# Kernel optimization log

Measured on AMD Instinct MI355X. Metric: run time of the kernel, lower is better.

## Reference

```python
import jax, jax.numpy as jnp
import numpy as np

E = 1024
H = 16
D = E // H  # head_dim = 64
B = 2
S = 2048


def setup_inputs() -> dict:
    key = jax.random.key(0)
    ks = jax.random.split(key, 8)
    sc = 0.02
    return {
        "x": jax.random.normal(ks[0], (B, S, E), jnp.float32),
        "rotation_params": jax.random.normal(ks[1], (E, E), jnp.float32) * sc,
        "entangle_params": jax.random.normal(ks[2], (E, E), jnp.float32) * sc,
        "qkv_w": jax.random.normal(ks[3], (3 * E, E), jnp.float32) * sc,
        "qkv_b": jax.random.normal(ks[4], (3 * E,), jnp.float32) * sc,
        "out_w": jax.random.normal(ks[5], (E, E), jnp.float32) * sc,
        "out_b": jax.random.normal(ks[6], (E,), jnp.float32) * sc,
    }


def reference(x, rotation_params, entangle_params, qkv_w, qkv_b, out_w, out_b):
    b, s, _ = x.shape
    # qkv projection (torch Linear: x @ W.T + b)
    qkv = jnp.einsum('bse,fe->bsf', x, qkv_w) + qkv_b
    q, k, v = jnp.split(qkv, 3, axis=-1)
    # extra rotation / entangle matmuls on q and k
    q = jnp.matmul(q, rotation_params)
    k = jnp.matmul(k, entangle_params)
    # split heads: (b, h, s, d)
    q = q.reshape(b, s, H, D).transpose(0, 2, 1, 3)
    k = k.reshape(b, s, H, D).transpose(0, 2, 1, 3)
    v = v.reshape(b, s, H, D).transpose(0, 2, 1, 3)
    scores = jnp.einsum('bhqd,bhkd->bhqk', q, k) / np.sqrt(D).astype(np.float32)
    attn = jax.nn.softmax(scores, axis=-1)  # dropout p=0.0 -> identity
    out = jnp.einsum('bhqk,bhkd->bhqd', attn, v)
    out = out.transpose(0, 2, 1, 3).reshape(b, s, E)
    out = jnp.einsum('bse,fe->bsf', out, out_w) + out_b
    return out + x
```

## Files before the change

### kernel.cpp

```cpp
#include <hip/hip_runtime.h>

#define US unsigned short
#define UC unsigned char

typedef __bf16 bf16x8 __attribute__((ext_vector_type(8)));
typedef float f32x4 __attribute__((ext_vector_type(4)));
typedef unsigned int u32x4 __attribute__((ext_vector_type(4)));
typedef unsigned short u16x4 __attribute__((ext_vector_type(4)));
typedef unsigned int uint2v __attribute__((ext_vector_type(2)));

#define ALPHA_Q 0.180336880111f

#if __has_builtin(__builtin_amdgcn_exp2f)
#define EXP2F(x) __builtin_amdgcn_exp2f(x)
#else
#define EXP2F(x) __expf(0.69314718f * (x))
#endif

static __device__ __forceinline__ US f2bf(float f) {
    union { float f; unsigned u; } v; v.f = f;
    unsigned r = v.u + 0x7fffu + ((v.u >> 16) & 1u);
    return (US)(r >> 16);
}
static __device__ __forceinline__ float bf2f(US h) {
    union { unsigned u; float f; } v; v.u = ((unsigned)h) << 16;
    return v.f;
}
static __device__ __forceinline__ f32x4 mfma16(bf16x8 a, bf16x8 b, f32x4 c) {
    return __builtin_amdgcn_mfma_f32_16x16x32_bf16(a, b, c, 0, 0, 0);
}
static __device__ __forceinline__ f32x4 mfma_fp8(long long a, long long b, f32x4 c) {
    return __builtin_amdgcn_mfma_f32_16x16x32_fp8_fp8(a, b, c, 0, 0, 0);
}
static __device__ __forceinline__ void gload16(const US* g, US* l) {
    __builtin_amdgcn_global_load_lds(
        (const __attribute__((address_space(1))) void*)g,
        (__attribute__((address_space(3))) void*)l, 16, 0, 0);
}
static __device__ __forceinline__ void gload16b(const UC* g, UC* l) {
    __builtin_amdgcn_global_load_lds(
        (const __attribute__((address_space(1))) void*)g,
        (__attribute__((address_space(3))) void*)l, 16, 0, 0);
}
static __device__ __forceinline__ void stf(float* p, float v) { *p = v; }
static __device__ __forceinline__ void stf(US* p, float v) { *p = f2bf(v); }

__global__ __launch_bounds__(256) void prep(
    const float* __restrict__ x, US* __restrict__ xb,
    const float* __restrict__ qkvw, US* __restrict__ wv,
    const float* __restrict__ outw, US* __restrict__ wo,
    const float* __restrict__ Rm, US* __restrict__ rt,
    const float* __restrict__ Em, US* __restrict__ et,
    US* __restrict__ wqT, US* __restrict__ wkT,
    const float* __restrict__ qkvb, float* __restrict__ b3)
{
    __shared__ float t[64][65];
    const int bx = blockIdx.x;
    if (bx < 6144) {
        int i = bx * 256 + threadIdx.x;
        const float* s; US* d; int j;
        if (i < 1048576) { s = x; d = xb; j = i; }
        else if (i < 1310720) { s = qkvw + (size_t)2048 * 1024; d = wv; j = i - 1048576; }
        else { s = outw; d = wo; j = i - 1310720; }
        f32x4 v = ((const f32x4*)s)[j];
        u16x4 o;
        o.x = f2bf(v.x); o.y = f2bf(v.y); o.z = f2bf(v.z); o.w = f2bf(v.w);
        ((u16x4*)d)[j] = o;
    } else if (bx < 7168) {
        int r = bx - 6144;
        int z = r >> 8, xy = r & 255, tbx = xy & 15, tby = xy >> 4;
        const float* ip; US* op;
        switch (z) {
            case 0: ip = Rm; op = rt; break;
            case 1: ip = Em; op = et; break;
            case 2: ip = qkvw; op = wqT; break;
            default: ip = qkvw + (size_t)1024 * 1024; op = wkT; break;
        }
        int bc = tbx * 64, br = tby * 64;
        int lx = threadIdx.x & 63, y4 = threadIdx.x >> 6;
#pragma unroll
        for (int i = 0; i < 16; ++i) {
            int rr = i * 4 + y4;
            t[rr][lx] = ip[(size_t)(br + rr) * 1024 + bc + lx];
        }
        __syncthreads();
#pragma unroll
        for (int i = 0; i < 16; ++i) {
            int c = i * 4 + y4;
            op[(size_t)(bc + c) * 1024 + br + lx] = f2bf(t[lx][c]);
        }
    } else if (bx < 7296) {
        float (*red)[64] = (float(*)[64])t;
        const int bb = bx - 7168;
        const int tid = threadIdx.x, wave = tid >> 6, lane = tid & 63;
        const int nc = bb & 31, jc = bb >> 5;
        const int n0 = nc * 64, n = n0 + lane;
        const float* M = (n0 < 1024) ? Rm : Em;
        const float* bv = qkvb + ((n0 < 1024) ? 0 : 1024);
        const int nn = (n0 < 1024) ? n : n - 1024;
        float s = 0.f;
        const int j0 = jc * 256 + wave * 64;
#pragma unroll 8
        for (int j = 0; j < 64; ++j)
            s += bv[j0 + j] * M[(size_t)(j0 + j) * 1024 + nn];
        red[wave][lane] = s;
        __syncthreads();
        if (wave == 0) {
            float tt = red[0][lane] + red[1][lane] + red[2][lane] + red[3][lane];
            atomicAdd(&b3[n], (n0 < 1024) ? tt * ALPHA_Q : tt);
        }
    } else {
        int i = (bx - 7296) * 256 + threadIdx.x;
        b3[2048 + i] = qkvb[2048 + i];
    }
}

template <typename TO>
__global__ __launch_bounds__(256) void gemm_nt64(
    const US* __restrict__ A, const US* __restrict__ Bm,
    TO* __restrict__ C, const float* __restrict__ bias,
    const float* __restrict__ resid,
    int M, int N, int K, int lda, int ldb, int ldc)
{
    __shared__ __align__(16) US sA[64 * 32];
    __shared__ __align__(16) US sB[128 * 32];
    const int tid = threadIdx.x;
    const int wave = tid >> 6, lane = tid & 63;
    const int r16 = lane & 15, q4 = lane >> 4;
    const int wm = (wave >> 1) * 32, wn = (wave & 1) * 64;

    const US* aptr = A + (size_t)(blockIdx.x * 64 + wave * 16 + (lane >> 2)) * lda + (lane & 3) * 8;
    const US* bptr = Bm + (size_t)(blockIdx.y * 128 + wave * 32 + (lane >> 2)) * ldb + (lane & 3) * 8;
    US* lA = sA + (wave * 16) * 32;
    US* lB = sB + (wave * 32) * 32;

    f32x4 acc[2][4];
#pragma unroll
    for (int i = 0; i < 2; ++i)
#pragma unroll
        for (int j = 0; j < 4; ++j) acc[i][j] = (f32x4){0.f, 0.f, 0.f, 0.f};

    for (int k0 = 0; k0 < K; k0 += 32) {
        gload16(aptr + k0, lA);
        gload16(bptr + k0, lB);
        gload16(bptr + (size_t)16 * ldb + k0, lB + 16 * 32);
        __syncthreads();
        bf16x8 af[2], bfr[4];
#pragma unroll
        for (int i = 0; i < 2; ++i)
            af[i] = *(const bf16x8*)&sA[(wm + i * 16 + r16) * 32 + q4 * 8];
#pragma unroll
        for (int j = 0; j < 4; ++j)
            bfr[j] = *(const bf16x8*)&sB[(wn + j * 16 + r16) * 32 + q4 * 8];
#pragma unroll
        for (int i = 0; i < 2; ++i)
#pragma unroll
            for (int j = 0; j < 4; ++j) acc[i][j] = mfma16(af[i], bfr[j], acc[i][j]);
        __syncthreads();
    }

#pragma unroll
    for (int j = 0; j < 4; ++j) {
        int col = blockIdx.y * 128 + wn + j * 16 + r16;
        float bv = bias ? bias[col] : 0.f;
#pragma unroll
        for (int i = 0; i < 2; ++i) {
#pragma unroll
            for (int rr = 0; rr < 4; ++rr) {
                int row = blockIdx.x * 64 + wm + i * 16 + q4 * 4 + rr;
                float v = acc[i][j][rr] + bv;
                if (resid) v += resid[(size_t)row * ldc + col];
                stf(&C[(size_t)row * ldc + col], v);
            }
        }
    }
}

__global__ __launch_bounds__(256) void gemm_qkv(
    const US* __restrict__ A, const US* __restrict__ Bm,
    const float* __restrict__ bias,
    US* __restrict__ qk, UC* __restrict__ vt)
{
    __shared__ __align__(16) US sA[64 * 32];
    __shared__ __align__(16) US sB[128 * 32];
    const int tid = threadIdx.x;
    const int wave = tid >> 6, lane = tid & 63;
    const int r16 = lane & 15, q4 = lane >> 4;
    const int wm = (wave >> 1) * 32, wn = (wave & 1) * 64;

    const US* aptr = A + (size_t)(blockIdx.x * 64 + wave * 16 + (lane >> 2)) * 1024 + (lane & 3) * 8;
    const US* bptr = Bm + (size_t)(blockIdx.y * 128 + wave * 32 + (lane >> 2)) * 1024 + (lane & 3) * 8;
    US* lA = sA + (wave * 16) * 32;
    US* lB = sB + (wave * 32) * 32;

    f32x4 acc[2][4];
#pragma unroll
    for (int i = 0; i < 2; ++i)
#pragma unroll
        for (int j = 0; j < 4; ++j) acc[i][j] = (f32x4){0.f, 0.f, 0.f, 0.f};

    for (int k0 = 0; k0 < 1024; k0 += 32) {
        gload16(aptr + k0, lA);
        gload16(bptr + k0, lB);
        gload16(bptr + (size_t)16 * 1024 + k0, lB + 16 * 32);
        __syncthreads();
        bf16x8 af[2], bfr[4];
#pragma unroll
        for (int i = 0; i < 2; ++i)
            af[i] = *(const bf16x8*)&sA[(wm + i * 16 + r16) * 32 + q4 * 8];
#pragma unroll
        for (int j = 0; j < 4; ++j)
            bfr[j] = *(const bf16x8*)&sB[(wn + j * 16 + r16) * 32 + q4 * 8];
#pragma unroll
        for (int i = 0; i < 2; ++i)
#pragma unroll
            for (int j = 0; j < 4; ++j) acc[i][j] = mfma16(af[i], bfr[j], acc[i][j]);
        __syncthreads();
    }

    if (blockIdx.y < 16) {
#pragma unroll
        for (int j = 0; j < 4; ++j) {
            int col = blockIdx.y * 128 + wn + j * 16 + r16;
            float bv = bias[col];
#pragma unroll
            for (int i = 0; i < 2; ++i)
#pragma unroll
                for (int rr = 0; rr < 4; ++rr) {
                    int row = blockIdx.x * 64 + wm + i * 16 + q4 * 4 + rr;
                    qk[(size_t)row * 2048 + col] = f2bf(acc[i][j][rr] + bv);
                }
        }
    } else {
#pragma unroll
        for (int j = 0; j < 4; ++j) {
            int col = blockIdx.y * 128 + wn + j * 16 + r16;
            float bv = bias[col];
            int f = col - 2048;
#pragma unroll
            for (int i = 0; i < 2; ++i) {
                int row0 = blockIdx.x * 64 + wm + i * 16 + q4 * 4;
                int b = row0 >> 11, s0 = row0 & 2047;
                int k = s0 & 63;
                int p = (s0 & ~63) | ((k & 24) << 1) | ((k & 32) >> 2) | (k & 7);
                int dw = __builtin_amdgcn_cvt_pk_fp8_f32(
                    acc[i][j][0] + bv, acc[i][j][1] + bv, 0, false);
                dw = __builtin_amdgcn_cvt_pk_fp8_f32(
                    acc[i][j][2] + bv, acc[i][j][3] + bv, dw, true);
                *(unsigned int*)&vt[((size_t)(b * 1024 + f)) * 2048 + p] = (unsigned)dw;
            }
        }
    }
}

__global__ __launch_bounds__(256) void gemm_fold(
    const US* __restrict__ rt, const US* __restrict__ wqT,
    const US* __restrict__ et, const US* __restrict__ wkT,
    US* __restrict__ comb)
{
    __shared__ __align__(16) US sA[64 * 32];
    __shared__ __align__(16) US sB[64 * 32];
    const US* A; const US* Bm; US* C; float alpha;
    if (blockIdx.z == 0) { A = rt; Bm = wqT; C = comb; alpha = ALPHA_Q; }
    else { A = et; Bm = wkT; C = comb + (size_t)1024 * 1024; alpha = 1.0f; }

    const int tid = threadIdx.x;
    const int wave = tid >> 6, lane = tid & 63;
    const int r16 = lane & 15, q4 = lane >> 4;
    const int wm = (wave >> 1) * 32, wn = (wave & 1) * 32;

    const int srow = wave * 16 + (lane >> 2);
    const int sg = lane & 3;
    const US* aptr = A + (size_t)(blockIdx.x * 64 + srow) * 1024 + sg * 8;
    const US* bptr = Bm + (size_t)(blockIdx.y * 64 + srow) * 1024 + sg * 8;
    US* lA = sA + (wave * 16) * 32;
    US* lB = sB + (wave * 16) * 32;

    f32x4 acc[2][2];
#pragma unroll
    for (int i = 0; i < 2; ++i)
#pragma unroll
        for (int j = 0; j < 2; ++j) acc[i][j] = (f32x4){0.f, 0.f, 0.f, 0.f};

    for (int k0 = 0; k0 < 1024; k0 += 32) {
        gload16(aptr + k0, lA);
        gload16(bptr + k0, lB);
        __syncthreads();
        bf16x8 af[2], bfr[2];
#pragma unroll
        for (int i = 0; i < 2; ++i)
            af[i] = *(const bf16x8*)&sA[(wm + i * 16 + r16) * 32 + q4 * 8];
#pragma unroll
        for (int j = 0; j < 2; ++j)
            bfr[j] = *(const bf16x8*)&sB[(wn + j * 16 + r16) * 32 + q4 * 8];
#pragma unroll
        for (int i = 0; i < 2; ++i)
#pragma unroll
            for (int j = 0; j < 2; ++j) acc[i][j] = mfma16(af[i], bfr[j], acc[i][j]);
        __syncthreads();
    }

#pragma unroll
    for (int j = 0; j < 2; ++j) {
        int col = blockIdx.y * 64 + wn + j * 16 + r16;
#pragma unroll
        for (int i = 0; i < 2; ++i)
#pragma unroll
            for (int rr = 0; rr < 4; ++rr) {
                int row = blockIdx.x * 64 + wm + i * 16 + q4 * 4 + rr;
                C[(size_t)row * 1024 + col] = f2bf(acc[i][j][rr] * alpha);
            }
    }
}

__global__ __launch_bounds__(256) void attn_kernel(
    const US* __restrict__ qk, const UC* __restrict__ vt, US* __restrict__ out)
{
    __shared__ __align__(16) US sK[2 * 64 * 64];
    __shared__ __align__(16) UC sV[2 * 64 * 64];
    __shared__ __align__(16) UC sP[64 * 72];
    __shared__ float lred[4][64];
    const int tid = threadIdx.x;
    const int wave = tid >> 6, lane = tid & 63;
    const int r16 = lane & 15, q4 = lane >> 4;
    const int bid = blockIdx.x;
    const int pair = (bid & 7) * 4 + ((bid >> 3) & 3);
    const int qc = bid >> 5;
    const int h = pair & 15, b = pair >> 4;
    const int qrow0 = qc * 64;
    const int c7 = r16 & 7;

    const US* qbase = qk + ((size_t)(b * 2048 + qrow0)) * 2048 + h * 64;
    bf16x8 qa[4][2];
#pragma unroll
    for (int qt = 0; qt < 4; ++qt)
#pragma unroll
        for (int kh = 0; kh < 2; ++kh)
            qa[qt][kh] = *(const bf16x8*)(qbase + (size_t)(qt * 16 + r16) * 2048 + kh * 32 + q4 * 8);

    f32x4 o[4];
    float lacc[4];
#pragma unroll
    for (int qt = 0; qt < 4; ++qt) { o[qt] = (f32x4){0.f, 0.f, 0.f, 0.f}; lacc[qt] = 0.f; }

    const int l8 = lane >> 3;
    const US* kg = qk + ((size_t)(b * 2048 + wave * 16 + l8)) * 2048 + 1024 + h * 64
                 + ((lane & 7) ^ l8) * 8;
    const int r4 = lane >> 2;
    const UC* vg = vt + ((size_t)((b * 16 + h) * 64 + wave * 16 + r4)) * 2048
                 + ((lane & 3) ^ (r4 & 3)) * 16;

#define STAGE(kc, buf) do {                                                    \
        US* dK = sK + (buf) * 4096 + (wave * 16) * 64;                         \
        UC* dV = sV + (buf) * 4096 + (wave * 16) * 64;                         \
        gload16(kg + (size_t)(kc) * 2048, dK);                                 \
        gload16(kg + (size_t)((kc) + 8) * 2048, dK + 8 * 64);                  \
        gload16b(vg + (kc), dV);                                               \
    } while (0)

    STAGE(0, 0);
    for (int it = 0; it < 32; ++it) {
        const int buf = it & 1;
        asm volatile("s_waitcnt vmcnt(0)" ::: "memory");
        asm volatile("s_barrier" ::: "memory");
        if (it < 31) STAGE((it + 1) * 64, buf ^ 1);

        const US* K0 = sK + buf * 4096;
        bf16x8 kf0 = *(const bf16x8*)&K0[(wave * 16 + r16) * 64 + ((0 + q4) ^ c7) * 8];
        bf16x8 kf1 = *(const bf16x8*)&K0[(wave * 16 + r16) * 64 + ((4 + q4) ^ c7) * 8];
#pragma unroll
        for (int qt = 0; qt < 4; ++qt) {
            f32x4 st = mfma16(kf0, qa[qt][0], (f32x4){0.f, 0.f, 0.f, 0.f});
            st = mfma16(kf1, qa[qt][1], st);
            float p0 = EXP2F(st[0]), p1 = EXP2F(st[1]);
            float p2 = EXP2F(st[2]), p3 = EXP2F(st[3]);
            lacc[qt] += (p0 + p1) + (p2 + p3);
            int dw = __builtin_amdgcn_cvt_pk_fp8_f32(p0, p1, 0, false);
            dw = __builtin_amdgcn_cvt_pk_fp8_f32(p2, p3, dw, true);
            *(unsigned int*)&sP[(qt * 16 + r16) * 72 + wave * 16 + q4 * 4] = (unsigned)dw;
        }
        asm volatile("s_waitcnt lgkmcnt(0)" ::: "memory");
        asm volatile("s_barrier" ::: "memory");

        const UC* V0 = sV + buf * 4096;
        u32x4 vv = *(const u32x4*)&V0[(wave * 16 + r16) * 64 + (q4 ^ (r16 & 3)) * 16];
        long long vf0, vf1;
        { uint2v t0 = {vv.x, vv.y}; vf0 = *(long long*)&t0; }
        { uint2v t1 = {vv.z, vv.w}; vf1 = *(long long*)&t1; }
#pragma unroll
        for (int qt = 0; qt < 4; ++qt) {
            long long pa0 = *(const long long*)&sP[(qt * 16 + r16) * 72 + q4 * 8];
            long long pa1 = *(const long long*)&sP[(qt * 16 + r16) * 72 + 32 + q4 * 8];
            o[qt] = mfma_fp8(vf0, pa0, o[qt]);
            o[qt] = mfma_fp8(vf1, pa1, o[qt]);
        }
    }
#undef STAGE

#pragma unroll
    for (int qt = 0; qt < 4; ++qt) {
        float l = lacc[qt];
        l += __shfl_xor(l, 16);
        l += __shfl_xor(l, 32);
        if (q4 == 0) lred[wave][qt * 16 + r16] = l;
    }
    __syncthreads();
#pragma unroll
    for (int qt = 0; qt < 4; ++qt) {
        int i = qt * 16 + r16;
        float l = lred[0][i] + lred[1][i] + lred[2][i] + lred[3][i];
        float inv = 1.0f / l;
        size_t row = (size_t)(b * 2048 + qrow0 + qt * 16 + r16);
        uint2v w;
        w.x = (unsigned)f2bf(o[qt][0] * inv) | ((unsigned)f2bf(o[qt][1] * inv) << 16);
        w.y = (unsigned)f2bf(o[qt][2] * inv) | ((unsigned)f2bf(o[qt][3] * inv) << 16);
        *(uint2v*)&out[row * 1024 + h * 64 + wave * 16 + q4 * 4] = w;
    }
}

extern "C" void kernel_launch(void* const* d_in, const int* in_sizes, int n_in,
                              void* d_out, int out_size, void* d_ws, size_t ws_size,
                              hipStream_t stream)
{
    const float* x    = (const float*)d_in[0];
    const float* Rm   = (const float*)d_in[1];
    const float* Em   = (const float*)d_in[2];
    const float* qkvw = (const float*)d_in[3];
    const float* qkvb = (const float*)d_in[4];
    const float* outw = (const float*)d_in[5];
    const float* outb = (const float*)d_in[6];
    float* outp = (float*)d_out;

    US* ws    = (US*)d_ws;
    US* xb    = ws;
    US* rt    = xb   + (size_t)4096 * 1024;
    US* et    = rt   + (size_t)1024 * 1024;
    US* wqT   = et   + (size_t)1024 * 1024;
    US* wkT   = wqT  + (size_t)1024 * 1024;
    US* wo    = wkT  + (size_t)1024 * 1024;
    US* comb  = wo   + (size_t)1024 * 1024;
    US* qkvq  = comb + (size_t)3072 * 1024;
    US* ao    = qkvq + (size_t)4096 * 2048;
    UC* vt    = (UC*)(ao + (size_t)4096 * 1024);
    float* b3 = (float*)(vt + (size_t)2048 * 2048);

    hipMemsetAsync(b3, 0, 2048 * sizeof(float), stream);
    prep<<<dim3(7300), dim3(256), 0, stream>>>(
        x, xb, qkvw, comb + (size_t)2048 * 1024, outw, wo,
        Rm, rt, Em, et, wqT, wkT, qkvb, b3);
    gemm_fold<<<dim3(16, 16, 2), dim3(256), 0, stream>>>(rt, wqT, et, wkT, comb);
    gemm_qkv<<<dim3(64, 24), dim3(256), 0, stream>>>(xb, comb, b3, qkvq, vt);
    attn_kernel<<<dim3(1024), dim3(256), 0, stream>>>(qkvq, vt, ao);
    gemm_nt64<float><<<dim3(64, 8), dim3(256), 0, stream>>>(ao, wo, outp, outb, x,
                                                            4096, 1024, 1024, 1024, 1024, 1024);
}
```

Baseline: 232.2 us.

## Double GEMM K-tile to 64 with XOR-swizzled LDS; compute softmax denominators via fp8 MFMA

Both bf16 GEMM kernels now stage 64-wide K slices instead of 32, using an XOR swizzle on the LDS column chunks to avoid bank conflicts. This halves the barrier count and issues more MFMAs per sync, at the cost of doubled shared memory. The attention kernel stops accumulating row sums of P in floats. Instead it sums the fp8-quantized P tile with an MFMA against a ones vector, one row block per wave, which removes the per-element adds and the cross-wave shuffle reduction. The denominator now matches the quantized values used in the PV product.

After: 212.5 us. 8.5% less time.

```diff
diff --git a/kernel.cpp b/kernel.cpp
--- a/kernel.cpp
+++ b/kernel.cpp
@@ -122,17 +122,17 @@
     const float* __restrict__ resid,
     int M, int N, int K, int lda, int ldb, int ldc)
 {
-    __shared__ __align__(16) US sA[64 * 32];
-    __shared__ __align__(16) US sB[128 * 32];
+    __shared__ __align__(16) US sA[64 * 64];
+    __shared__ __align__(16) US sB[128 * 64];
     const int tid = threadIdx.x;
     const int wave = tid >> 6, lane = tid & 63;
     const int r16 = lane & 15, q4 = lane >> 4;
     const int wm = (wave >> 1) * 32, wn = (wave & 1) * 64;
-
-    const US* aptr = A + (size_t)(blockIdx.x * 64 + wave * 16 + (lane >> 2)) * lda + (lane & 3) * 8;
-    const US* bptr = Bm + (size_t)(blockIdx.y * 128 + wave * 32 + (lane >> 2)) * ldb + (lane & 3) * 8;
-    US* lA = sA + (wave * 16) * 32;
-    US* lB = sB + (wave * 32) * 32;
+    const int c7 = r16 & 7;
+
+    const int l8 = lane >> 3, lg = (lane & 7) ^ l8;
+    const US* aptr = A + (size_t)(blockIdx.x * 64 + wave * 16 + l8) * lda + lg * 8;
+    const US* bptr = Bm + (size_t)(blockIdx.y * 128 + wave * 32 + l8) * ldb + lg * 8;
 
     f32x4 acc[2][4];
 #pragma unroll
@@ -140,22 +140,31 @@
 #pragma unroll
         for (int j = 0; j < 4; ++j) acc[i][j] = (f32x4){0.f, 0.f, 0.f, 0.f};
 
-    for (int k0 = 0; k0 < K; k0 += 32) {
-        gload16(aptr + k0, lA);
-        gload16(bptr + k0, lB);
-        gload16(bptr + (size_t)16 * ldb + k0, lB + 16 * 32);
-        __syncthreads();
-        bf16x8 af[2], bfr[4];
-#pragma unroll
-        for (int i = 0; i < 2; ++i)
-            af[i] = *(const bf16x8*)&sA[(wm + i * 16 + r16) * 32 + q4 * 8];
+    for (int k0 = 0; k0 < K; k0 += 64) {
+        gload16(aptr + k0, sA + (wave * 16) * 64);
+        gload16(aptr + (size_t)8 * lda + k0, sA + (wave * 16 + 8) * 64);
+#pragma unroll
+        for (int c = 0; c < 4; ++c)
+            gload16(bptr + (size_t)(c * 8) * ldb + k0, sB + (wave * 32 + c * 8) * 64);
+        __syncthreads();
+        bf16x8 af[2][2], bfr[4][2];
+#pragma unroll
+        for (int i = 0; i < 2; ++i)
+#pragma unroll
+            for (int hf = 0; hf < 2; ++hf)
+                af[i][hf] = *(const bf16x8*)&sA[(wm + i * 16 + r16) * 64 + ((hf * 4 + q4) ^ c7) * 8];
 #pragma unroll
         for (int j = 0; j < 4; ++j)
-            bfr[j] = *(const bf16x8*)&sB[(wn + j * 16 + r16) * 32 + q4 * 8];
-#pragma unroll
-        for (int i = 0; i < 2; ++i)
-#pragma unroll
-            for (int j = 0; j < 4; ++j) acc[i][j] = mfma16(af[i], bfr[j], acc[i][j]);
+#pragma unroll
+            for (int hf = 0; hf < 2; ++hf)
+                bfr[j][hf] = *(const bf16x8*)&sB[(wn + j * 16 + r16) * 64 + ((hf * 4 + q4) ^ c7) * 8];
+#pragma unroll
+        for (int i = 0; i < 2; ++i)
+#pragma unroll
+            for (int j = 0; j < 4; ++j) {
+                acc[i][j] = mfma16(af[i][0], bfr[j][0], acc[i][j]);
+                acc[i][j] = mfma16(af[i][1], bfr[j][1], acc[i][j]);
+            }
         __syncthreads();
     }
 
@@ -181,17 +190,17 @@
     const float* __restrict__ bias,
     US* __restrict__ qk, UC* __restrict__ vt)
 {
-    __shared__ __align__(16) US sA[64 * 32];
-    __shared__ __align__(16) US sB[128 * 32];
+    __shared__ __align__(16) US sA[64 * 64];
+    __shared__ __align__(16) US sB[128 * 64];
     const int tid = threadIdx.x;
     const int wave = tid >> 6, lane = tid & 63;
     const int r16 = lane & 15, q4 = lane >> 4;
     const int wm = (wave >> 1) * 32, wn = (wave & 1) * 64;
-
-    const US* aptr = A + (size_t)(blockIdx.x * 64 + wave * 16 + (lane >> 2)) * 1024 + (lane & 3) * 8;
-    const US* bptr = Bm + (size_t)(blockIdx.y * 128 + wave * 32 + (lane >> 2)) * 1024 + (lane & 3) * 8;
-    US* lA = sA + (wave * 16) * 32;
-    US* lB = sB + (wave * 32) * 32;
+    const int c7 = r16 & 7;
+
+    const int l8 = lane >> 3, lg = (lane & 7) ^ l8;
+    const US* aptr = A + (size_t)(blockIdx.x * 64 + wave * 16 + l8) * 1024 + lg * 8;
+    const US* bptr = Bm + (size_t)(blockIdx.y * 128 + wave * 32 + l8) * 1024 + lg * 8;
 
     f32x4 acc[2][4];
 #pragma unroll
@@ -199,22 +208,31 @@
 #pragma unroll
         for (int j = 0; j < 4; ++j) acc[i][j] = (f32x4){0.f, 0.f, 0.f, 0.f};
 
-    for (int k0 = 0; k0 < 1024; k0 += 32) {
-        gload16(aptr + k0, lA);
-        gload16(bptr + k0, lB);
-        gload16(bptr + (size_t)16 * 1024 + k0, lB + 16 * 32);
-        __syncthreads();
-        bf16x8 af[2], bfr[4];
-#pragma unroll
-        for (int i = 0; i < 2; ++i)
-            af[i] = *(const bf16x8*)&sA[(wm + i * 16 + r16) * 32 + q4 * 8];
+    for (int k0 = 0; k0 < 1024; k0 += 64) {
+        gload16(aptr + k0, sA + (wave * 16) * 64);
+        gload16(aptr + (size_t)8 * 1024 + k0, sA + (wave * 16 + 8) * 64);
+#pragma unroll
+        for (int c = 0; c < 4; ++c)
+            gload16(bptr + (size_t)(c * 8) * 1024 + k0, sB + (wave * 32 + c * 8) * 64);
+        __syncthreads();
+        bf16x8 af[2][2], bfr[4][2];
+#pragma unroll
+        for (int i = 0; i < 2; ++i)
+#pragma unroll
+            for (int hf = 0; hf < 2; ++hf)
+                af[i][hf] = *(const bf16x8*)&sA[(wm + i * 16 + r16) * 64 + ((hf * 4 + q4) ^ c7) * 8];
 #pragma unroll
         for (int j = 0; j < 4; ++j)
-            bfr[j] = *(const bf16x8*)&sB[(wn + j * 16 + r16) * 32 + q4 * 8];
-#pragma unroll
-        for (int i = 0; i < 2; ++i)
-#pragma unroll
-            for (int j = 0; j < 4; ++j) acc[i][j] = mfma16(af[i], bfr[j], acc[i][j]);
+#pragma unroll
+            for (int hf = 0; hf < 2; ++hf)
+                bfr[j][hf] = *(const bf16x8*)&sB[(wn + j * 16 + r16) * 64 + ((hf * 4 + q4) ^ c7) * 8];
+#pragma unroll
+        for (int i = 0; i < 2; ++i)
+#pragma unroll
+            for (int j = 0; j < 4; ++j) {
+                acc[i][j] = mfma16(af[i][0], bfr[j][0], acc[i][j]);
+                acc[i][j] = mfma16(af[i][1], bfr[j][1], acc[i][j]);
+            }
         __syncthreads();
     }
 
@@ -319,7 +337,7 @@
     __shared__ __align__(16) US sK[2 * 64 * 64];
     __shared__ __align__(16) UC sV[2 * 64 * 64];
     __shared__ __align__(16) UC sP[64 * 72];
-    __shared__ float lred[4][64];
+    __shared__ float lred[64];
     const int tid = threadIdx.x;
     const int wave = tid >> 6, lane = tid & 63;
     const int r16 = lane & 15, q4 = lane >> 4;
@@ -329,6 +347,7 @@
     const int h = pair & 15, b = pair >> 4;
     const int qrow0 = qc * 64;
     const int c7 = r16 & 7;
+    const long long ones8 = 0x3838383838383838LL;
 
     const US* qbase = qk + ((size_t)(b * 2048 + qrow0)) * 2048 + h * 64;
     bf16x8 qa[4][2];
@@ -339,9 +358,10 @@
             qa[qt][kh] = *(const bf16x8*)(qbase + (size_t)(qt * 16 + r16) * 2048 + kh * 32 + q4 * 8);
 
     f32x4 o[4];
-    float lacc[4];
-#pragma unroll
-    for (int qt = 0; qt < 4; ++qt) { o[qt] = (f32x4){0.f, 0.f, 0.f, 0.f}; lacc[qt] = 0.f; }
+    f32x4 lC;
+#pragma unroll
+    for (int qt = 0; qt < 4; ++qt) o[qt] = (f32x4){0.f, 0.f, 0.f, 0.f};
+    lC = (f32x4){0.f, 0.f, 0.f, 0.f};
 
     const int l8 = lane >> 3;
     const US* kg = qk + ((size_t)(b * 2048 + wave * 16 + l8)) * 2048 + 1024 + h * 64
@@ -374,7 +394,6 @@
             st = mfma16(kf1, qa[qt][1], st);
             float p0 = EXP2F(st[0]), p1 = EXP2F(st[1]);
             float p2 = EXP2F(st[2]), p3 = EXP2F(st[3]);
-            lacc[qt] += (p0 + p1) + (p2 + p3);
             int dw = __builtin_amdgcn_cvt_pk_fp8_f32(p0, p1, 0, false);
             dw = __builtin_amdgcn_cvt_pk_fp8_f32(p2, p3, dw, true);
             *(unsigned int*)&sP[(qt * 16 + r16) * 72 + wave * 16 + q4 * 4] = (unsigned)dw;
@@ -394,22 +413,20 @@
             o[qt] = mfma_fp8(vf0, pa0, o[qt]);
             o[qt] = mfma_fp8(vf1, pa1, o[qt]);
         }
+        {
+            long long pl0 = *(const long long*)&sP[(wave * 16 + r16) * 72 + q4 * 8];
+            long long pl1 = *(const long long*)&sP[(wave * 16 + r16) * 72 + 32 + q4 * 8];
+            lC = mfma_fp8(ones8, pl0, lC);
+            lC = mfma_fp8(ones8, pl1, lC);
+        }
     }
 #undef STAGE
 
+    if (q4 == 0) lred[wave * 16 + r16] = lC[0];
+    __syncthreads();
 #pragma unroll
     for (int qt = 0; qt < 4; ++qt) {
-        float l = lacc[qt];
-        l += __shfl_xor(l, 16);
-        l += __shfl_xor(l, 32);
-        if (q4 == 0) lred[wave][qt * 16 + r16] = l;
-    }
-    __syncthreads();
-#pragma unroll
-    for (int qt = 0; qt < 4; ++qt) {
-        int i = qt * 16 + r16;
-        float l = lred[0][i] + lred[1][i] + lred[2][i] + lred[3][i];
-        float inv = 1.0f / l;
+        float inv = 1.0f / lred[qt * 16 + r16];
         size_t row = (size_t)(b * 2048 + qrow0 + qt * 16 + r16);
         uint2v w;
         w.x = (unsigned)f2bf(o[qt][0] * inv) | ((unsigned)f2bf(o[qt][1] * inv) << 16);
```
